# Optimization experiments

Hardware: AMD Instinct MI355X
Metric: run time of the kernel (lower is better)

## Reference

```python
import jax, jax.numpy as jnp
import numpy as np

# Config / sizes
N = 20000       # nodes
E = 320000      # edges (avg degree 16)
IN_DIM = 6      # node feature dim
PE = 8          # laplacian PE dims
ED = 4          # edge feature dim
H = 128         # hidden dim
OUT = 4         # output dim
L = 3           # message-passing layers
T = 3           # node types (typed encoders/decoders)


def mlp(z, W1, b1, W2, b2):
    # _make_mlp: Linear -> ReLU -> Linear
    return jax.nn.relu(z @ W1 + b1) @ W2 + b2


def typed_mlp(z, W1, b1, W2, b2, types):
    # W1: [T, Din, H]; compute all T branches, select per-node by type
    h = jax.nn.relu(jnp.einsum('ni,tih->tnh', z, W1) + b1[:, None, :])
    o = jnp.einsum('tnh,tho->tno', h, W2) + b2[:, None, :]
    onehot = jax.nn.one_hot(types, W1.shape[0], dtype=o.dtype)  # [N, T]
    return jnp.einsum('tno,nt->no', o, onehot)


def setup_inputs() -> dict:
    key = jax.random.key(0)
    ks = jax.random.split(key, 40)

    def w(k, shape, fan_in):
        return jax.random.normal(k, shape, dtype=jnp.float32) / np.float32(np.sqrt(fan_in))

    inp = {}
    inp['x'] = jax.random.normal(ks[0], (N, IN_DIM), dtype=jnp.float32)
    inp['pe'] = jax.random.normal(ks[1], (N, PE), dtype=jnp.float32)
    inp['edge_attr'] = jax.random.normal(ks[2], (E, ED), dtype=jnp.float32)
    # typed node encoders: (in_dim+pe_dims) -> H -> H
    inp['enc_W1'] = w(ks[3], (T, IN_DIM + PE, H), IN_DIM + PE)
    inp['enc_b1'] = jnp.zeros((T, H), jnp.float32)
    inp['enc_W2'] = w(ks[4], (T, H, H), H)
    inp['enc_b2'] = jnp.zeros((T, H), jnp.float32)
    # edge encoder: ED -> H -> H
    inp['ee_W1'] = w(ks[5], (ED, H), ED)
    inp['ee_b1'] = jnp.zeros((H,), jnp.float32)
    inp['ee_W2'] = w(ks[6], (H, H), H)
    inp['ee_b2'] = jnp.zeros((H,), jnp.float32)
    # per-layer edge update (3H->H->H), node update (2H->H->H), fusion (H->H->H)
    inp['eu_W1'] = w(ks[7], (L, 3 * H, H), 3 * H)
    inp['eu_b1'] = jnp.zeros((L, H), jnp.float32)
    inp['eu_W2'] = w(ks[8], (L, H, H), H)
    inp['eu_b2'] = jnp.zeros((L, H), jnp.float32)
    inp['nu_W1'] = w(ks[9], (L, 2 * H, H), 2 * H)
    inp['nu_b1'] = jnp.zeros((L, H), jnp.float32)
    inp['nu_W2'] = w(ks[10], (L, H, H), H)
    inp['nu_b2'] = jnp.zeros((L, H), jnp.float32)
    inp['fu_W1'] = w(ks[11], (L, H, H), H)
    inp['fu_b1'] = jnp.zeros((L, H), jnp.float32)
    inp['fu_W2'] = w(ks[12], (L, H, H), H)
    inp['fu_b2'] = jnp.zeros((L, H), jnp.float32)
    # typed decoders: H -> H -> OUT
    inp['dec_W1'] = w(ks[13], (T, H, H), H)
    inp['dec_b1'] = jnp.zeros((T, H), jnp.float32)
    inp['dec_W2'] = w(ks[14], (T, H, OUT), H)
    inp['dec_b2'] = jnp.zeros((T, OUT), jnp.float32)
    # int inputs
    inp['edge_index'] = jax.random.randint(ks[15], (2, E), 0, N)
    inp['node_types'] = jax.random.randint(ks[16], (N,), 0, T)
    return inp


def reference(x, pe, edge_attr,
              enc_W1, enc_b1, enc_W2, enc_b2,
              ee_W1, ee_b1, ee_W2, ee_b2,
              eu_W1, eu_b1, eu_W2, eu_b2,
              nu_W1, nu_b1, nu_W2, nu_b2,
              fu_W1, fu_b1, fu_W2, fu_b2,
              dec_W1, dec_b1, dec_W2, dec_b2,
              edge_index, node_types):
    n = x.shape[0]
    src, dst = edge_index[0], edge_index[1]
    # typed node encode on [x || pe]
    h_nodes = typed_mlp(jnp.concatenate([x, pe], axis=-1),
                        enc_W1, enc_b1, enc_W2, enc_b2, node_types)
    # edge encode
    h_edges = mlp(edge_attr, ee_W1, ee_b1, ee_W2, ee_b2)
    num_layers = eu_W1.shape[0]
    for l in range(num_layers):
        # gather endpoint states, edge MLP, residual on edges
        m_edge = mlp(jnp.concatenate([h_nodes[src], h_nodes[dst], h_edges], axis=-1),
                     eu_W1[l], eu_b1[l], eu_W2[l], eu_b2[l])
        h_edges = h_edges + m_edge
        # scatter-add aggregation to destination nodes (index_add_)
        m_node = jax.ops.segment_sum(h_edges, dst, num_segments=n)
        # node update + residual, then fusion (dropout is eval/identity)
        upd = mlp(jnp.concatenate([h_nodes, m_node], axis=-1),
                  nu_W1[l], nu_b1[l], nu_W2[l], nu_b2[l])
        local = h_nodes + upd
        h_nodes = mlp(local, fu_W1[l], fu_b1[l], fu_W2[l], fu_b2[l])
    # typed decode
    out = typed_mlp(h_nodes, dec_W1, dec_b1, dec_W2, dec_b2, node_types)
    return out
```

## Files before the change

### kernel.cpp

```cpp
#include <hip/hip_runtime.h>
#include <hip/hip_bf16.h>

typedef __hip_bfloat16 bf16;
typedef __attribute__((ext_vector_type(8))) short short8;
typedef __attribute__((ext_vector_type(4))) float floatx4;

#define HDIM 128
#define NCANON 27

__device__ __forceinline__ float b2f(bf16 v) { return __bfloat162float(v); }
__device__ __forceinline__ float s2f(short s) {
  return __uint_as_float(((unsigned int)(unsigned short)s) << 16);
}
__device__ __forceinline__ short f2s(float f) {
  return (short)__bfloat16_as_ushort(__float2bfloat16(f));
}

struct CanonDesc {
  const void* src[NCANON];
  int prefix[NCANON + 1];
};

__global__ void canon_kernel(CanonDesc d, const unsigned short* __restrict__ xraw,
                             int* __restrict__ flagOut, bf16* __restrict__ out, int total) {
  __shared__ int sflag;
  int tid = threadIdx.x;
  if (tid < 64) {
    unsigned short u = xraw[2 * tid];
    int e = (u >> 7) & 0xFF;
    int ok = (u == 0) || (e >= 100 && e <= 140);
    unsigned long long m = __ballot(ok);
    if (tid == 0) sflag = (__popcll(m) >= 48) ? 1 : 0;
  }
  __syncthreads();
  int isBf = sflag;
  if (blockIdx.x == 0 && tid == 0) flagOut[0] = isBf;
  int t = blockIdx.x * 256 + tid;
  if (t >= total) return;
  int lo = 0, hi = NCANON;
  while (lo + 1 < hi) { int mid = (lo + hi) >> 1; if (d.prefix[mid] <= t) lo = mid; else hi = mid; }
  int off = t - d.prefix[lo];
  out[t] = isBf ? ((const bf16*)d.src[lo])[off]
                : __float2bfloat16(((const float*)d.src[lo])[off]);
}

__global__ void hist_kernel(const int* __restrict__ dst, int* __restrict__ cnt, int E) {
  int e = blockIdx.x * 256 + threadIdx.x;
  if (e < E) atomicAdd(&cnt[dst[e]], 1);
}

__global__ void scan1_kernel(const int* __restrict__ cnt, int* __restrict__ bsum, int n) {
  int tid = threadIdx.x, lane = tid & 63, wave = tid >> 6;
  int i = blockIdx.x * 256 + tid;
  int v = (i < n) ? cnt[i] : 0;
  #pragma unroll
  for (int d = 32; d; d >>= 1) v += __shfl_down(v, d);
  __shared__ int ws[4];
  if (lane == 0) ws[wave] = v;
  __syncthreads();
  if (tid == 0) bsum[blockIdx.x] = ws[0] + ws[1] + ws[2] + ws[3];
}

__global__ void scan2_kernel(int* __restrict__ bsum, int nb) {
  int lane = threadIdx.x;
  int a0 = (lane < nb) ? bsum[lane] : 0;
  int b0 = (64 + lane < nb) ? bsum[64 + lane] : 0;
  int a = a0, b = b0;
  #pragma unroll
  for (int d = 1; d < 64; d <<= 1) { int t = __shfl_up(a, d); if (lane >= d) a += t; }
  int totA = __shfl(a, 63);
  #pragma unroll
  for (int d = 1; d < 64; d <<= 1) { int t = __shfl_up(b, d); if (lane >= d) b += t; }
  int totB = __shfl(b, 63);
  if (lane < nb) bsum[lane] = a - a0;
  if (64 + lane < nb) bsum[64 + lane] = b - b0 + totA;
  if (lane == 0) bsum[nb] = totA + totB;
}

__global__ void scan3_kernel(const int* __restrict__ cnt, const int* __restrict__ bsum,
                             int* __restrict__ row_start, int n, int nb) {
  __shared__ int sh[256];
  int tid = threadIdx.x;
  int i = blockIdx.x * 256 + tid;
  int v = (i < n) ? cnt[i] : 0;
  sh[tid] = v;
  __syncthreads();
  #pragma unroll
  for (int off = 1; off < 256; off <<= 1) {
    int t = (tid >= off) ? sh[tid - off] : 0;
    __syncthreads();
    sh[tid] += t;
    __syncthreads();
  }
  if (i < n) row_start[i] = bsum[blockIdx.x] + sh[tid] - v;
  if (blockIdx.x == 0 && tid == 0) row_start[n] = bsum[nb];
}

__global__ void scatter_kernel(const int* __restrict__ src, const int* __restrict__ dst,
                               const int* __restrict__ row_start, int* __restrict__ cursor,
                               const bf16* __restrict__ ea, bf16* __restrict__ eaS,
                               int* __restrict__ srcS, int* __restrict__ dstS, int E) {
  int e = blockIdx.x * 256 + threadIdx.x;
  if (e < E) {
    int d = dst[e];
    int pos = row_start[d] + atomicAdd(&cursor[d], 1);
    srcS[pos] = src[e];
    dstS[pos] = d;
    *(uint2*)(eaS + (size_t)pos * 4) = *(const uint2*)(ea + (size_t)e * 4);
  }
}

__global__ void __launch_bounds__(1024) tsort_kernel(const int* __restrict__ types,
                                                     int* __restrict__ ts,
                                                     int* __restrict__ perm, int n) {
  __shared__ int wc[16][3];
  __shared__ int base[3];
  int tid = threadIdx.x, lane = tid & 63, wave = tid >> 6;
  int c0 = 0, c1 = 0, c2 = 0;
  for (int i = tid; i < n; i += 1024) {
    int t = types[i];
    c0 += (t == 0); c1 += (t == 1); c2 += (t == 2);
  }
  #pragma unroll
  for (int d = 32; d; d >>= 1) {
    c0 += __shfl_down(c0, d); c1 += __shfl_down(c1, d); c2 += __shfl_down(c2, d);
  }
  if (lane == 0) { wc[wave][0] = c0; wc[wave][1] = c1; wc[wave][2] = c2; }
  __syncthreads();
  if (tid == 0) {
    int t0 = 0, t1 = 0;
    for (int w = 0; w < 16; w++) { t0 += wc[w][0]; t1 += wc[w][1]; }
    ts[0] = 0; ts[1] = t0; ts[2] = t0 + t1; ts[3] = n;
    base[0] = 0; base[1] = t0; base[2] = t0 + t1;
  }
  __syncthreads();
  for (int i0 = 0; i0 < n; i0 += 1024) {
    int i = i0 + tid;
    int t = (i < n) ? types[i] : -1;
    unsigned long long m0 = __ballot(t == 0);
    unsigned long long m1 = __ballot(t == 1);
    unsigned long long m2 = __ballot(t == 2);
    if (lane == 0) { wc[wave][0] = __popcll(m0); wc[wave][1] = __popcll(m1); wc[wave][2] = __popcll(m2); }
    __syncthreads();
    if (i < n) {
      unsigned long long mt = (t == 0) ? m0 : ((t == 1) ? m1 : m2);
      unsigned long long below = (lane == 0) ? 0ull : ((1ull << lane) - 1ull);
      int r = __popcll(mt & below);
      int woff = 0;
      for (int w = 0; w < wave; w++) woff += wc[w][t];
      perm[base[t] + woff + r] = i;
    }
    __syncthreads();
    if (tid == 0) {
      int a0 = 0, a1 = 0, a2 = 0;
      for (int w = 0; w < 16; w++) { a0 += wc[w][0]; a1 += wc[w][1]; a2 += wc[w][2]; }
      base[0] += a0; base[1] += a1; base[2] += a2;
    }
    __syncthreads();
  }
}

struct PackJob { const bf16* src; bf16* dst; int Ksrc; int KS; int srcCols; };
struct PackJobs { PackJob j[40]; };

__global__ void pack_all_kernel(PackJobs J) {
  PackJob job = J.j[blockIdx.y];
  int idx = blockIdx.x * 256 + threadIdx.x;
  int total = 8 * job.KS * 64;
  if (idx >= total) return;
  int lane = idx & 63;
  int ks = (idx >> 6) % job.KS;
  int ct = idx / (64 * job.KS);
  bf16* o = job.dst + (size_t)idx * 8;
  int ncol = ct * 16 + (lane & 15);
  int kb = ks * 32 + ((lane >> 4) & 3) * 8;
  #pragma unroll
  for (int jj = 0; jj < 8; jj++) {
    int k = kb + jj;
    o[jj] = (k < job.Ksrc && ncol < job.srcCols)
              ? job.src[(size_t)k * job.srcCols + ncol] : __float2bfloat16(0.f);
  }
}

__global__ void __launch_bounds__(256) ygemm_kernel(
    const bf16* __restrict__ X,
    const bf16* __restrict__ WpA, const bf16* __restrict__ WpB,
    bf16* __restrict__ outA, bf16* __restrict__ outB,
    float* __restrict__ mnode, int M) {
  const bf16* Wp = blockIdx.y ? WpB : WpA;
  bf16* outp = blockIdx.y ? outB : outA;
  constexpr int BM = 64, RT = 4, SK = 136;
  __shared__ bf16 Zt[BM * SK];
  const int tid = threadIdx.x;
  const int lane = tid & 63, wave = tid >> 6, colq = lane & 15, quad = lane >> 4;
  const int row0 = blockIdx.x * BM;
  if (blockIdx.y == 0) {
    float4 z = {0.f, 0.f, 0.f, 0.f};
    for (int i = tid; i < BM * 32; i += 256) {
      int row = i >> 5, q = i & 31;
      int gr = row0 + row;
      if (gr < M) *(float4*)(mnode + (size_t)gr * HDIM + q * 4) = z;
    }
  }
  {
    int row = tid >> 2, sub = tid & 3;
    int gr = row0 + row;
    bool ok = gr < M;
    #pragma unroll
    for (int j = 0; j < 4; j++) {
      int seg = j * 4 + sub;
      uint4 v = {0u, 0u, 0u, 0u};
// ... 307 lines not shown
    }
  }
  #pragma unroll
  for (int c = 0; c < 2; c++) {
    int col = wave * 32 + c * 16 + colq;
    float bv = b2f(fuB2[col]);
    #pragma unroll
    for (int rt = 0; rt < RT; rt++)
      #pragma unroll
      for (int r = 0; r < 4; r++) {
        int lrow = rt * 16 + quad * 4 + r;
        int grow = row0 + lrow;
        bf16 hb = __float2bfloat16(acc[rt][c][r] + bv);
        Zt[lrow * SK + col] = hb;
        if (grow < M) outp[(size_t)grow * HDIM + col] = hb;
      }
  }
  if (!yW1a) return;
  __syncthreads();

  #pragma unroll
  for (int which = 0; which < 2; which++) {
    const bf16* Wp = which ? yW1b : yW1a;
    bf16* outy = which ? ysB : ysA;
    #pragma unroll
    for (int rt = 0; rt < RT; rt++)
      #pragma unroll
      for (int c = 0; c < 2; c++) acc[rt][c] = (floatx4){0.f, 0.f, 0.f, 0.f};
    #pragma unroll
    for (int ks = 0; ks < 4; ks++) {
      short8 bfr0 = *(const short8*)(Wp + (((size_t)(wave * 2 + 0) * 4 + ks) * 64 + lane) * 8);
      short8 bfr1 = *(const short8*)(Wp + (((size_t)(wave * 2 + 1) * 4 + ks) * 64 + lane) * 8);
      #pragma unroll
      for (int rt = 0; rt < RT; rt++) {
        short8 a = *(const short8*)(&Zt[(rt * 16 + colq) * SK + ks * 32 + quad * 8]);
        acc[rt][0] = __builtin_amdgcn_mfma_f32_16x16x32_bf16(a, bfr0, acc[rt][0], 0, 0, 0);
        acc[rt][1] = __builtin_amdgcn_mfma_f32_16x16x32_bf16(a, bfr1, acc[rt][1], 0, 0, 0);
      }
    }
    #pragma unroll
    for (int c = 0; c < 2; c++) {
      int col = wave * 32 + c * 16 + colq;
      #pragma unroll
      for (int rt = 0; rt < RT; rt++)
        #pragma unroll
        for (int r = 0; r < 4; r++) {
          int grow = row0 + rt * 16 + quad * 4 + r;
          if (grow < M) outy[(size_t)grow * HDIM + col] = __float2bfloat16(acc[rt][c][r]);
        }
    }
  }
}

template<int KS1, bool DEC>
__global__ void __launch_bounds__(256) typed_kernel(
    const bf16* __restrict__ in0, const bf16* __restrict__ in1,
    const int* __restrict__ perm, const int* __restrict__ ts, const int* __restrict__ flagp,
    const bf16* __restrict__ W1p, int w1s, const bf16* __restrict__ b1v, int b1s,
    const bf16* __restrict__ W2p, int w2s, const bf16* __restrict__ b2v, int b2s,
    void* __restrict__ outp) {
  constexpr int BM = 64, RT = 4;
  constexpr int SK = KS1 * 32 + 8;
  constexpr int HS = 136;
  int t = blockIdx.y;
  int rs = ts[t], re = ts[t + 1];
  int row0 = rs + blockIdx.x * BM;
  if (row0 >= re) return;
  __shared__ bf16 Zt[BM * SK];
  __shared__ bf16 Hid[BM * HS];
  __shared__ int gIdx[BM];
  const int tid = threadIdx.x;
  const int lane = tid & 63, wave = tid >> 6, colq = lane & 15, quad = lane >> 4;
  for (int i = tid; i < BM; i += 256) gIdx[i] = (row0 + i < re) ? perm[row0 + i] : -1;
  __syncthreads();
  if (DEC) {
    int row = tid >> 2, sub = tid & 3;
    int g = gIdx[row];
    #pragma unroll
    for (int j = 0; j < 4; j++) {
      int seg = j * 4 + sub;
      uint4 v = {0u, 0u, 0u, 0u};
      if (g >= 0) v = *(const uint4*)(in0 + (size_t)g * HDIM + seg * 8);
      *(uint4*)(&Zt[row * SK + seg * 8]) = v;
    }
  } else {
    for (int i = tid; i < BM * 32; i += 256) {
      int row = i >> 5, k = i & 31;
      int g = gIdx[row];
      bf16 v = __float2bfloat16(0.f);
      if (g >= 0 && k < 14) v = (k < 6) ? in0[(size_t)g * 6 + k] : in1[(size_t)g * 8 + (k - 6)];
      Zt[row * SK + k] = v;
    }
  }
  __syncthreads();

  const bf16* W1t = W1p + (size_t)t * w1s;
  const bf16* W2t = W2p + (size_t)t * w2s;
  floatx4 acc[RT][2];
  #pragma unroll
  for (int rt = 0; rt < RT; rt++)
    #pragma unroll
    for (int c = 0; c < 2; c++) acc[rt][c] = (floatx4){0.f, 0.f, 0.f, 0.f};
  #pragma unroll
  for (int ks = 0; ks < KS1; ks++) {
    short8 bfr0 = *(const short8*)(W1t + (((size_t)(wave * 2 + 0) * KS1 + ks) * 64 + lane) * 8);
    short8 bfr1 = *(const short8*)(W1t + (((size_t)(wave * 2 + 1) * KS1 + ks) * 64 + lane) * 8);
    #pragma unroll
    for (int rt = 0; rt < RT; rt++) {
      short8 a = *(const short8*)(&Zt[(rt * 16 + colq) * SK + ks * 32 + quad * 8]);
      acc[rt][0] = __builtin_amdgcn_mfma_f32_16x16x32_bf16(a, bfr0, acc[rt][0], 0, 0, 0);
      acc[rt][1] = __builtin_amdgcn_mfma_f32_16x16x32_bf16(a, bfr1, acc[rt][1], 0, 0, 0);
    }
  }
  #pragma unroll
  for (int c = 0; c < 2; c++) {
    int col = wave * 32 + c * 16 + colq;
    float bv = b2f(b1v[t * b1s + col]);
    #pragma unroll
    for (int rt = 0; rt < RT; rt++)
      #pragma unroll
      for (int r = 0; r < 4; r++) {
        float v = acc[rt][c][r] + bv;
        Hid[(rt * 16 + quad * 4 + r) * HS + col] = __float2bfloat16(fmaxf(v, 0.f));
      }
  }
  __syncthreads();

  floatx4 acc2[RT][2];
  #pragma unroll
  for (int rt = 0; rt < RT; rt++)
    #pragma unroll
    for (int c = 0; c < 2; c++) acc2[rt][c] = (floatx4){0.f, 0.f, 0.f, 0.f};
  #pragma unroll
  for (int ks = 0; ks < 4; ks++) {
    short8 bfr0 = *(const short8*)(W2t + (((size_t)(wave * 2 + 0) * 4 + ks) * 64 + lane) * 8);
    short8 bfr1 = *(const short8*)(W2t + (((size_t)(wave * 2 + 1) * 4 + ks) * 64 + lane) * 8);
    #pragma unroll
    for (int rt = 0; rt < RT; rt++) {
      short8 a = *(const short8*)(&Hid[(rt * 16 + colq) * HS + ks * 32 + quad * 8]);
      acc2[rt][0] = __builtin_amdgcn_mfma_f32_16x16x32_bf16(a, bfr0, acc2[rt][0], 0, 0, 0);
      acc2[rt][1] = __builtin_amdgcn_mfma_f32_16x16x32_bf16(a, bfr1, acc2[rt][1], 0, 0, 0);
    }
  }
  if (DEC) {
    if (wave == 0 && colq < 4) {
      int isBf = flagp[0];
      float bv = b2f(b2v[t * b2s + colq]);
      #pragma unroll
      for (int rt = 0; rt < RT; rt++)
        #pragma unroll
        for (int r = 0; r < 4; r++) {
          int g = gIdx[rt * 16 + quad * 4 + r];
          if (g >= 0) {
            float v = acc2[rt][0][r] + bv;
            if (isBf) ((bf16*)outp)[(size_t)g * 4 + colq] = __float2bfloat16(v);
            else      ((float*)outp)[(size_t)g * 4 + colq] = v;
          }
        }
    }
  } else {
    #pragma unroll
    for (int c = 0; c < 2; c++) {
      int col = wave * 32 + c * 16 + colq;
      float bv = b2f(b2v[t * b2s + col]);
      #pragma unroll
      for (int rt = 0; rt < RT; rt++)
        #pragma unroll
        for (int r = 0; r < 4; r++) {
          int g = gIdx[rt * 16 + quad * 4 + r];
          if (g >= 0) ((bf16*)outp)[(size_t)g * HDIM + col] = __float2bfloat16(acc2[rt][c][r] + bv);
        }
    }
  }
}

template<int BM>
__global__ void __launch_bounds__(256) ee_kernel(
    const bf16* __restrict__ eaS,
    const bf16* __restrict__ W1p, const bf16* __restrict__ b1v,
    const bf16* __restrict__ W2p, const bf16* __restrict__ b2v,
    bf16* __restrict__ outp, int M) {
  constexpr int RT = BM / 16;
  constexpr int SK = 136;
  __shared__ bf16 Zt[BM * SK];
  const int tid = threadIdx.x;
  const int lane = tid & 63, wave = tid >> 6, colq = lane & 15, quad = lane >> 4;
  const int row0 = blockIdx.x * BM;

  for (int i = tid; i < BM * 4; i += 256) {
    int row = i >> 2, seg = i & 3;
    int gr = row0 + row;
    uint4 val = {0u, 0u, 0u, 0u};
    if (seg == 0 && gr < M) {
      uint2 v = *(const uint2*)(eaS + (size_t)gr * 4);
      val.x = v.x; val.y = v.y;
    }
    *(uint4*)(&Zt[row * SK + seg * 8]) = val;
  }
  __syncthreads();

  floatx4 acc[RT][2];
  #pragma unroll
  for (int rt = 0; rt < RT; rt++)
    #pragma unroll
    for (int c = 0; c < 2; c++) acc[rt][c] = (floatx4){0.f, 0.f, 0.f, 0.f};
  {
    short8 bfr0 = *(const short8*)(W1p + (((size_t)(wave * 2 + 0)) * 64 + lane) * 8);
    short8 bfr1 = *(const short8*)(W1p + (((size_t)(wave * 2 + 1)) * 64 + lane) * 8);
    #pragma unroll
    for (int rt = 0; rt < RT; rt++) {
      short8 a = *(const short8*)(&Zt[(rt * 16 + colq) * SK + quad * 8]);
      acc[rt][0] = __builtin_amdgcn_mfma_f32_16x16x32_bf16(a, bfr0, acc[rt][0], 0, 0, 0);
      acc[rt][1] = __builtin_amdgcn_mfma_f32_16x16x32_bf16(a, bfr1, acc[rt][1], 0, 0, 0);
    }
  }
  __syncthreads();
  #pragma unroll
  for (int c = 0; c < 2; c++) {
    int col = wave * 32 + c * 16 + colq;
    float bv = b2f(b1v[col]);
    #pragma unroll
    for (int rt = 0; rt < RT; rt++)
      #pragma unroll
      for (int r = 0; r < 4; r++)
        Zt[(rt * 16 + quad * 4 + r) * SK + col] =
            __float2bfloat16(fmaxf(acc[rt][c][r] + bv, 0.f));
  }
  __syncthreads();

  floatx4 acc2[RT][2];
  #pragma unroll
  for (int rt = 0; rt < RT; rt++)
    #pragma unroll
    for (int c = 0; c < 2; c++) acc2[rt][c] = (floatx4){0.f, 0.f, 0.f, 0.f};
  #pragma unroll
  for (int ks = 0; ks < 4; ks++) {
    short8 bfr0 = *(const short8*)(W2p + (((size_t)(wave * 2 + 0) * 4 + ks) * 64 + lane) * 8);
    short8 bfr1 = *(const short8*)(W2p + (((size_t)(wave * 2 + 1) * 4 + ks) * 64 + lane) * 8);
    #pragma unroll
    for (int rt = 0; rt < RT; rt++) {
      short8 a = *(const short8*)(&Zt[(rt * 16 + colq) * SK + ks * 32 + quad * 8]);
      acc2[rt][0] = __builtin_amdgcn_mfma_f32_16x16x32_bf16(a, bfr0, acc2[rt][0], 0, 0, 0);
      acc2[rt][1] = __builtin_amdgcn_mfma_f32_16x16x32_bf16(a, bfr1, acc2[rt][1], 0, 0, 0);
    }
  }
  #pragma unroll
  for (int c = 0; c < 2; c++) {
    int col = wave * 32 + c * 16 + colq;
    float bv = b2f(b2v[col]);
    #pragma unroll
    for (int rt = 0; rt < RT; rt++)
      #pragma unroll
      for (int r = 0; r < 4; r++) {
        int grow = row0 + rt * 16 + quad * 4 + r;
        if (grow < M)
          outp[(size_t)grow * HDIM + col] = __float2bfloat16(acc2[rt][c][r] + bv);
      }
  }
}

extern "C" void kernel_launch(void* const* d_in, const int* in_sizes, int n_in,
                              void* d_out, int out_size, void* d_ws, size_t ws_size,
                              hipStream_t stream) {
  const int* edge_index = (const int*)d_in[27];
  const int* node_types = (const int*)d_in[28];
  const int N = in_sizes[28];
  const int E = in_sizes[2] / 4;
  const int L = in_sizes[12] / HDIM;
  const int* srcI = edge_index;
  const int* dstI = edge_index + E;

  CanonDesc cd;
  int total = 0;
  for (int i = 0; i < NCANON; i++) { cd.src[i] = d_in[i]; cd.prefix[i] = total; total += in_sizes[i]; }
  cd.prefix[NCANON] = total;

  char* wsb = (char*)d_ws;
  size_t off = 0;
  auto alloc = [&](size_t bytes) -> void* {
    void* p = wsb + off;
    off += (bytes + 255) & ~(size_t)255;
    return p;
  };
  int*  flag      = (int*)alloc(256);
  bf16* arena     = (bf16*)alloc((size_t)total * 2);
  bf16* h_nodes   = (bf16*)alloc((size_t)N * HDIM * 2);
  bf16* h_edges   = (bf16*)alloc((size_t)E * HDIM * 2);
  float* m_node   = (float*)alloc((size_t)N * HDIM * 4);
  bf16* ysrcb     = (bf16*)alloc((size_t)N * HDIM * 2);
  bf16* ydstb     = (bf16*)alloc((size_t)N * HDIM * 2);
  bf16* eaS       = (bf16*)alloc((size_t)E * 4 * 2);
  int* counts     = (int*)alloc((size_t)N * 4);
  int* cursor     = (int*)alloc((size_t)N * 4);
  int* row_start  = (int*)alloc((size_t)(N + 1) * 4);
  int* bsum       = (int*)alloc(260 * 4);
  int* srcS       = (int*)alloc((size_t)E * 4);
  int* dstS       = (int*)alloc((size_t)E * 4);
  int* tsArr      = (int*)alloc(64);
  int* permT      = (int*)alloc((size_t)N * 4);
  bf16* eeW1p  = (bf16*)alloc(4096 * 2);
  bf16* eeW2p  = (bf16*)alloc(16384 * 2);
  bf16* encW1p = (bf16*)alloc(3 * 4096 * 2);
  bf16* encW2p = (bf16*)alloc(3 * 16384 * 2);
  bf16* decW1p = (bf16*)alloc(3 * 16384 * 2);
  bf16* decW2p = (bf16*)alloc(3 * 16384 * 2);
  bf16* euW1a  = (bf16*)alloc((size_t)L * 16384 * 2);
  bf16* euW1b  = (bf16*)alloc((size_t)L * 16384 * 2);
  bf16* euW1c  = (bf16*)alloc((size_t)L * 16384 * 2);
  bf16* euW2p  = (bf16*)alloc((size_t)L * 16384 * 2);
  bf16* nuW1p  = (bf16*)alloc((size_t)L * 32768 * 2);
  bf16* nuW2p  = (bf16*)alloc((size_t)L * 16384 * 2);
  bf16* fuW1p  = (bf16*)alloc((size_t)L * 16384 * 2);
  bf16* fuW2p  = (bf16*)alloc((size_t)L * 16384 * 2);

  const bf16* cX     = arena + cd.prefix[0];
  const bf16* cPE    = arena + cd.prefix[1];
  const bf16* cEA    = arena + cd.prefix[2];
  const bf16* cEncW1 = arena + cd.prefix[3];
  const bf16* cEncB1 = arena + cd.prefix[4];
  const bf16* cEncW2 = arena + cd.prefix[5];
  const bf16* cEncB2 = arena + cd.prefix[6];
  const bf16* cEeW1  = arena + cd.prefix[7];
  const bf16* cEeB1  = arena + cd.prefix[8];
  const bf16* cEeW2  = arena + cd.prefix[9];
  const bf16* cEeB2  = arena + cd.prefix[10];
  const bf16* cEuW1  = arena + cd.prefix[11];
  const bf16* cEuB1  = arena + cd.prefix[12];
  const bf16* cEuW2  = arena + cd.prefix[13];
  const bf16* cEuB2  = arena + cd.prefix[14];
  const bf16* cNuW1  = arena + cd.prefix[15];
  const bf16* cNuB1  = arena + cd.prefix[16];
  const bf16* cNuW2  = arena + cd.prefix[17];
  const bf16* cNuB2  = arena + cd.prefix[18];
  const bf16* cFuW1  = arena + cd.prefix[19];
  const bf16* cFuB1  = arena + cd.prefix[20];
  const bf16* cFuW2  = arena + cd.prefix[21];
  const bf16* cFuB2  = arena + cd.prefix[22];
  const bf16* cDecW1 = arena + cd.prefix[23];
  const bf16* cDecB1 = arena + cd.prefix[24];
  const bf16* cDecW2 = arena + cd.prefix[25];
  const bf16* cDecB2 = arena + cd.prefix[26];

  canon_kernel<<<(total + 255) / 256, 256, 0, stream>>>(
      cd, (const unsigned short*)d_in[0], flag, arena, total);

  hipMemsetAsync(counts, 0, (size_t)N * 4, stream);
  hipMemsetAsync(cursor, 0, (size_t)N * 4, stream);

  PackJobs PJ;
  int nj = 0;
  PJ.j[nj++] = {cEeW1, eeW1p, 4, 1, 128};
  PJ.j[nj++] = {cEeW2, eeW2p, 128, 4, 128};
  for (int l = 0; l < L; l++) {
    const bf16* w1 = cEuW1 + (size_t)l * 384 * HDIM;
    PJ.j[nj++] = {w1,                 euW1a + (size_t)l * 16384, 128, 4, 128};
    PJ.j[nj++] = {w1 + 128 * HDIM,    euW1b + (size_t)l * 16384, 128, 4, 128};
    PJ.j[nj++] = {w1 + 256 * HDIM,    euW1c + (size_t)l * 16384, 128, 4, 128};
    PJ.j[nj++] = {cEuW2 + (size_t)l * HDIM * HDIM, euW2p + (size_t)l * 16384, 128, 4, 128};
    PJ.j[nj++] = {cNuW1 + (size_t)l * 256 * HDIM,  nuW1p + (size_t)l * 32768, 256, 8, 128};
    PJ.j[nj++] = {cNuW2 + (size_t)l * HDIM * HDIM, nuW2p + (size_t)l * 16384, 128, 4, 128};
    PJ.j[nj++] = {cFuW1 + (size_t)l * HDIM * HDIM, fuW1p + (size_t)l * 16384, 128, 4, 128};
    PJ.j[nj++] = {cFuW2 + (size_t)l * HDIM * HDIM, fuW2p + (size_t)l * 16384, 128, 4, 128};
  }
  for (int t = 0; t < 3; t++) {
    PJ.j[nj++] = {cEncW1 + (size_t)t * 14 * HDIM,   encW1p + (size_t)t * 4096, 14, 1, 128};
    PJ.j[nj++] = {cEncW2 + (size_t)t * HDIM * HDIM, encW2p + (size_t)t * 16384, 128, 4, 128};
    PJ.j[nj++] = {cDecW1 + (size_t)t * HDIM * HDIM, decW1p + (size_t)t * 16384, 128, 4, 128};
    PJ.j[nj++] = {cDecW2 + (size_t)t * HDIM * 4,    decW2p + (size_t)t * 16384, 128, 4, 4};
  }
  pack_all_kernel<<<dim3(16, nj), 256, 0, stream>>>(PJ);

  int nb = (N + 255) / 256;
  hist_kernel<<<(E + 255) / 256, 256, 0, stream>>>(dstI, counts, E);
  scan1_kernel<<<nb, 256, 0, stream>>>(counts, bsum, N);
  scan2_kernel<<<1, 64, 0, stream>>>(bsum, nb);
  scan3_kernel<<<nb, 256, 0, stream>>>(counts, bsum, row_start, N, nb);
  scatter_kernel<<<(E + 255) / 256, 256, 0, stream>>>(srcI, dstI, row_start, cursor,
                                                      cEA, eaS, srcS, dstS, E);
  tsort_kernel<<<1, 1024, 0, stream>>>(node_types, tsArr, permT, N);

  int ngrid64 = (N + 63) / 64;
  typed_kernel<1, false><<<dim3(ngrid64, 3), 256, 0, stream>>>(
      cX, cPE, permT, tsArr, flag, encW1p, 4096, cEncB1, HDIM,
      encW2p, 16384, cEncB2, HDIM, h_nodes);

  int egrid32  = (E + 31) / 32;
  int egrid128 = (E + 127) / 128;

  ee_kernel<128><<<egrid128, 256, 0, stream>>>(
      eaS, eeW1p, cEeB1, eeW2p, cEeB2, h_edges, E);

  for (int l = 0; l < L; l++) {
    if (l == 0) {
      ygemm_kernel<<<dim3(ngrid64, 2), 256, 0, stream>>>(
          h_nodes, euW1a, euW1b, ysrcb, ydstb, m_node, N);
    }
    if (l + 1 < L) {
      eu_kernel<32, true><<<egrid32, 256, 0, stream>>>(
          h_edges, ysrcb, ydstb, srcS, dstS,
          euW1c + (size_t)l * 16384, cEuB1 + l * HDIM,
          euW2p + (size_t)l * 16384, cEuB2 + l * HDIM, h_edges, m_node, E);
    } else {
      eu_kernel<32, false><<<egrid32, 256, 0, stream>>>(
          h_edges, ysrcb, ydstb, srcS, dstS,
          euW1c + (size_t)l * 16384, cEuB1 + l * HDIM,
          euW2p + (size_t)l * 16384, cEuB2 + l * HDIM, h_edges, m_node, E);
    }
    bool hasNext = (l + 1 < L);
    node_kernel<<<ngrid64, 256, 0, stream>>>(
        h_nodes, m_node,
        nuW1p + (size_t)l * 32768, cNuB1 + l * HDIM,
        nuW2p + (size_t)l * 16384, cNuB2 + l * HDIM,
        fuW1p + (size_t)l * 16384, cFuB1 + l * HDIM,
        fuW2p + (size_t)l * 16384, cFuB2 + l * HDIM,
        hasNext ? euW1a + (size_t)(l + 1) * 16384 : nullptr,
        hasNext ? euW1b + (size_t)(l + 1) * 16384 : nullptr,
        ysrcb, ydstb, h_nodes, N);
  }

  typed_kernel<4, true><<<dim3(ngrid64, 3), 256, 0, stream>>>(
      h_nodes, nullptr, permT, tsArr, flag, decW1p, 16384, cDecB1, HDIM,
      decW2p, 16384, cDecB2, 4, d_out);
  (void)n_in; (void)ws_size;
}
```

Baseline: 476.2 us.

## Merge small setup kernels to cut launch count and dead work

Folds the memsets of counts and cursor into extra blocks of the canon kernel, merges the histogram with the type-sort kernel, and merges the edge encoder with the typed node encoder into one launch by splitting on block index. The decoder gets its own kernel whose second GEMM computes only the single 16-column tile that holds the 4 outputs, instead of 8 tiles where most were discarded. The aim is to remove launch gaps and serialization between small kernels, at the cost of more complex, branchy kernels. The zeroing relies on counts and cursor sitting contiguously in the workspace, and the large shared array in the merged encoder kernel may lower occupancy for the node-encode blocks.

```diff
diff --git a/kernel.cpp b/kernel.cpp
--- a/kernel.cpp
+++ b/kernel.cpp
@@ -22,9 +22,15 @@
 };
 
 __global__ void canon_kernel(CanonDesc d, const unsigned short* __restrict__ xraw,
-                             int* __restrict__ flagOut, bf16* __restrict__ out, int total) {
+                             int* __restrict__ flagOut, bf16* __restrict__ out, int total,
+                             int canonBlocks, uint4* __restrict__ zbase, int zquads) {
+  int tid = threadIdx.x;
+  if (blockIdx.x >= canonBlocks) {
+    int i = (blockIdx.x - canonBlocks) * 256 + tid;
+    if (i < zquads) { uint4 z = {0u, 0u, 0u, 0u}; zbase[i] = z; }
+    return;
+  }
   __shared__ int sflag;
-  int tid = threadIdx.x;
   if (tid < 64) {
     unsigned short u = xraw[2 * tid];
     int e = (u >> 7) & 0xFF;
@@ -44,75 +50,14 @@
                 : __float2bfloat16(((const float*)d.src[lo])[off]);
 }
 
-__global__ void hist_kernel(const int* __restrict__ dst, int* __restrict__ cnt, int E) {
-  int e = blockIdx.x * 256 + threadIdx.x;
-  if (e < E) atomicAdd(&cnt[dst[e]], 1);
-}
-
-__global__ void scan1_kernel(const int* __restrict__ cnt, int* __restrict__ bsum, int n) {
-  int tid = threadIdx.x, lane = tid & 63, wave = tid >> 6;
-  int i = blockIdx.x * 256 + tid;
-  int v = (i < n) ? cnt[i] : 0;
-  #pragma unroll
-  for (int d = 32; d; d >>= 1) v += __shfl_down(v, d);
-  __shared__ int ws[4];
-  if (lane == 0) ws[wave] = v;
-  __syncthreads();
-  if (tid == 0) bsum[blockIdx.x] = ws[0] + ws[1] + ws[2] + ws[3];
-}
-
-__global__ void scan2_kernel(int* __restrict__ bsum, int nb) {
-  int lane = threadIdx.x;
-  int a0 = (lane < nb) ? bsum[lane] : 0;
-  int b0 = (64 + lane < nb) ? bsum[64 + lane] : 0;
-  int a = a0, b = b0;
-  #pragma unroll
-  for (int d = 1; d < 64; d <<= 1) { int t = __shfl_up(a, d); if (lane >= d) a += t; }
-  int totA = __shfl(a, 63);
-  #pragma unroll
-  for (int d = 1; d < 64; d <<= 1) { int t = __shfl_up(b, d); if (lane >= d) b += t; }
-  int totB = __shfl(b, 63);
-  if (lane < nb) bsum[lane] = a - a0;
-  if (64 + lane < nb) bsum[64 + lane] = b - b0 + totA;
-  if (lane == 0) bsum[nb] = totA + totB;
-}
-
-__global__ void scan3_kernel(const int* __restrict__ cnt, const int* __restrict__ bsum,
-                             int* __restrict__ row_start, int n, int nb) {
-  __shared__ int sh[256];
-  int tid = threadIdx.x;
-  int i = blockIdx.x * 256 + tid;
-  int v = (i < n) ? cnt[i] : 0;
-  sh[tid] = v;
-  __syncthreads();
-  #pragma unroll
-  for (int off = 1; off < 256; off <<= 1) {
-    int t = (tid >= off) ? sh[tid - off] : 0;
-    __syncthreads();
-    sh[tid] += t;
-    __syncthreads();
-  }
-  if (i < n) row_start[i] = bsum[blockIdx.x] + sh[tid] - v;
-  if (blockIdx.x == 0 && tid == 0) row_start[n] = bsum[nb];
-}
-
-__global__ void scatter_kernel(const int* __restrict__ src, const int* __restrict__ dst,
-                               const int* __restrict__ row_start, int* __restrict__ cursor,
-                               const bf16* __restrict__ ea, bf16* __restrict__ eaS,
-                               int* __restrict__ srcS, int* __restrict__ dstS, int E) {
-  int e = blockIdx.x * 256 + threadIdx.x;
-  if (e < E) {
-    int d = dst[e];
-    int pos = row_start[d] + atomicAdd(&cursor[d], 1);
-    srcS[pos] = src[e];
-    dstS[pos] = d;
-    *(uint2*)(eaS + (size_t)pos * 4) = *(const uint2*)(ea + (size_t)e * 4);
-  }
-}
-
-__global__ void __launch_bounds__(1024) tsort_kernel(const int* __restrict__ types,
-                                                     int* __restrict__ ts,
-                                                     int* __restrict__ perm, int n) {
+__global__ void __launch_bounds__(1024) hist_tsort_kernel(
+    const int* __restrict__ dst, int* __restrict__ cnt, int E, int hb,
+    const int* __restrict__ types, int* __restrict__ ts, int* __restrict__ perm, int n) {
+  if (blockIdx.x < hb) {
+    int e = blockIdx.x * 1024 + threadIdx.x;
+    if (e < E) atomicAdd(&cnt[dst[e]], 1);
+    return;
+  }
   __shared__ int wc[16][3];
   __shared__ int base[3];
   int tid = threadIdx.x, lane = tid & 63, wave = tid >> 6;
@@ -157,6 +102,67 @@
       base[0] += a0; base[1] += a1; base[2] += a2;
     }
     __syncthreads();
+  }
+}
+
+__global__ void scan1_kernel(const int* __restrict__ cnt, int* __restrict__ bsum, int n) {
+  int tid = threadIdx.x, lane = tid & 63, wave = tid >> 6;
+  int i = blockIdx.x * 256 + tid;
+  int v = (i < n) ? cnt[i] : 0;
+  #pragma unroll
+  for (int d = 32; d; d >>= 1) v += __shfl_down(v, d);
+  __shared__ int ws[4];
+  if (lane == 0) ws[wave] = v;
+  __syncthreads();
+  if (tid == 0) bsum[blockIdx.x] = ws[0] + ws[1] + ws[2] + ws[3];
+}
+
+__global__ void scan2_kernel(int* __restrict__ bsum, int nb) {
+  int lane = threadIdx.x;
+  int a0 = (lane < nb) ? bsum[lane] : 0;
+  int b0 = (64 + lane < nb) ? bsum[64 + lane] : 0;
+  int a = a0, b = b0;
+  #pragma unroll
+  for (int d = 1; d < 64; d <<= 1) { int t = __shfl_up(a, d); if (lane >= d) a += t; }
+  int totA = __shfl(a, 63);
+  #pragma unroll
+  for (int d = 1; d < 64; d <<= 1) { int t = __shfl_up(b, d); if (lane >= d) b += t; }
+  int totB = __shfl(b, 63);
+  if (lane < nb) bsum[lane] = a - a0;
+  if (64 + lane < nb) bsum[64 + lane] = b - b0 + totA;
+  if (lane == 0) bsum[nb] = totA + totB;
+}
+
+__global__ void scan3_kernel(const int* __restrict__ cnt, const int* __restrict__ bsum,
+                             int* __restrict__ row_start, int n, int nb) {
+  __shared__ int sh[256];
+  int tid = threadIdx.x;
+  int i = blockIdx.x * 256 + tid;
+  int v = (i < n) ? cnt[i] : 0;
+  sh[tid] = v;
+  __syncthreads();
+  #pragma unroll
+  for (int off = 1; off < 256; off <<= 1) {
+    int t = (tid >= off) ? sh[tid - off] : 0;
+    __syncthreads();
+    sh[tid] += t;
+    __syncthreads();
+  }
+  if (i < n) row_start[i] = bsum[blockIdx.x] + sh[tid] - v;
+  if (blockIdx.x == 0 && tid == 0) row_start[n] = bsum[nb];
+}
+
+__global__ void scatter_kernel(const int* __restrict__ src, const int* __restrict__ dst,
+                               const int* __restrict__ row_start, int* __restrict__ cursor,
+                               const bf16* __restrict__ ea, bf16* __restrict__ eaS,
+                               int* __restrict__ srcS, int* __restrict__ dstS, int E) {
+  int e = blockIdx.x * 256 + threadIdx.x;
+  if (e < E) {
+    int d = dst[e];
+    int pos = row_start[d] + atomicAdd(&cursor[d], 1);
+    srcS[pos] = src[e];
+    dstS[pos] = d;
+    *(uint2*)(eaS + (size_t)pos * 4) = *(const uint2*)(ea + (size_t)e * 4);
   }
 }
 
@@ -570,16 +576,184 @@
   }
 }
 
-template<int KS1, bool DEC>
-__global__ void __launch_bounds__(256) typed_kernel(
-    const bf16* __restrict__ in0, const bf16* __restrict__ in1,
+__global__ void __launch_bounds__(256) encee_kernel(
+    int eeBlocks, int ngrid64,
+    const bf16* __restrict__ eaS,
+    const bf16* __restrict__ eeW1, const bf16* __restrict__ eeB1,
+    const bf16* __restrict__ eeW2, const bf16* __restrict__ eeB2,
+    bf16* __restrict__ h_edges, int E,
+    const bf16* __restrict__ x, const bf16* __restrict__ pe,
+    const int* __restrict__ perm, const int* __restrict__ ts,
+    const bf16* __restrict__ encW1, const bf16* __restrict__ encB1,
+    const bf16* __restrict__ encW2, const bf16* __restrict__ encB2,
+    bf16* __restrict__ h_nodes) {
+  __shared__ bf16 smem[128 * 136];
+  __shared__ int gIdx[64];
+  const int tid = threadIdx.x;
+  const int lane = tid & 63, wave = tid >> 6, colq = lane & 15, quad = lane >> 4;
+
+  if (blockIdx.x < eeBlocks) {
+    constexpr int BM = 128, RT = 8, SK = 136;
+    bf16* Zt = smem;
+    const int row0 = blockIdx.x * BM;
+    for (int i = tid; i < BM * 4; i += 256) {
+      int row = i >> 2, seg = i & 3;
+      int gr = row0 + row;
+      uint4 val = {0u, 0u, 0u, 0u};
+      if (seg == 0 && gr < E) {
+        uint2 v = *(const uint2*)(eaS + (size_t)gr * 4);
+        val.x = v.x; val.y = v.y;
+      }
+      *(uint4*)(&Zt[row * SK + seg * 8]) = val;
+    }
+    __syncthreads();
+    floatx4 acc[RT][2];
+    #pragma unroll
+    for (int rt = 0; rt < RT; rt++)
+      #pragma unroll
+      for (int c = 0; c < 2; c++) acc[rt][c] = (floatx4){0.f, 0.f, 0.f, 0.f};
+    {
+      short8 bfr0 = *(const short8*)(eeW1 + (((size_t)(wave * 2 + 0)) * 64 + lane) * 8);
+      short8 bfr1 = *(const short8*)(eeW1 + (((size_t)(wave * 2 + 1)) * 64 + lane) * 8);
+      #pragma unroll
+      for (int rt = 0; rt < RT; rt++) {
+        short8 a = *(const short8*)(&Zt[(rt * 16 + colq) * SK + quad * 8]);
+        acc[rt][0] = __builtin_amdgcn_mfma_f32_16x16x32_bf16(a, bfr0, acc[rt][0], 0, 0, 0);
+        acc[rt][1] = __builtin_amdgcn_mfma_f32_16x16x32_bf16(a, bfr1, acc[rt][1], 0, 0, 0);
+      }
+    }
+    __syncthreads();
+    #pragma unroll
+    for (int c = 0; c < 2; c++) {
+      int col = wave * 32 + c * 16 + colq;
+      float bv = b2f(eeB1[col]);
+      #pragma unroll
+      for (int rt = 0; rt < RT; rt++)
+        #pragma unroll
+        for (int r = 0; r < 4; r++)
+          Zt[(rt * 16 + quad * 4 + r) * SK + col] =
+              __float2bfloat16(fmaxf(acc[rt][c][r] + bv, 0.f));
+    }
+    __syncthreads();
+    floatx4 acc2[RT][2];
+    #pragma unroll
+    for (int rt = 0; rt < RT; rt++)
+      #pragma unroll
+      for (int c = 0; c < 2; c++) acc2[rt][c] = (floatx4){0.f, 0.f, 0.f, 0.f};
+    #pragma unroll
+    for (int ks = 0; ks < 4; ks++) {
+      short8 bfr0 = *(const short8*)(eeW2 + (((size_t)(wave * 2 + 0) * 4 + ks) * 64 + lane) * 8);
+      short8 bfr1 = *(const short8*)(eeW2 + (((size_t)(wave * 2 + 1) * 4 + ks) * 64 + lane) * 8);
+      #pragma unroll
+      for (int rt = 0; rt < RT; rt++) {
+        short8 a = *(const short8*)(&Zt[(rt * 16 + colq) * SK + ks * 32 + quad * 8]);
+        acc2[rt][0] = __builtin_amdgcn_mfma_f32_16x16x32_bf16(a, bfr0, acc2[rt][0], 0, 0, 0);
+        acc2[rt][1] = __builtin_amdgcn_mfma_f32_16x16x32_bf16(a, bfr1, acc2[rt][1], 0, 0, 0);
+      }
+    }
+    #pragma unroll
+    for (int c = 0; c < 2; c++) {
+      int col = wave * 32 + c * 16 + colq;
+      float bv = b2f(eeB2[col]);
+      #pragma unroll
+      for (int rt = 0; rt < RT; rt++)
+        #pragma unroll
+        for (int r = 0; r < 4; r++) {
+          int grow = row0 + rt * 16 + quad * 4 + r;
+          if (grow < E)
+            h_edges[(size_t)grow * HDIM + col] = __float2bfloat16(acc2[rt][c][r] + bv);
+        }
+    }
+    return;
+  }
+
+  {
+    constexpr int BM = 64, RT = 4, SK = 40, HS = 136;
+    bf16* Zt = smem;
+    bf16* Hid = smem + BM * SK;
+    int idx = blockIdx.x - eeBlocks;
+    int t = idx / ngrid64;
+    int bx = idx - t * ngrid64;
+    int rs = ts[t], re = ts[t + 1];
+    int row0 = rs + bx * BM;
+    if (row0 >= re) return;
+    for (int i = tid; i < BM; i += 256) gIdx[i] = (row0 + i < re) ? perm[row0 + i] : -1;
+    __syncthreads();
+    for (int i = tid; i < BM * 32; i += 256) {
+      int row = i >> 5, k = i & 31;
+      int g = gIdx[row];
+      bf16 v = __float2bfloat16(0.f);
+      if (g >= 0 && k < 14) v = (k < 6) ? x[(size_t)g * 6 + k] : pe[(size_t)g * 8 + (k - 6)];
+      Zt[row * SK + k] = v;
+    }
+    __syncthreads();
+    const bf16* W1t = encW1 + (size_t)t * 4096;
+    const bf16* W2t = encW2 + (size_t)t * 16384;
+    floatx4 acc[RT][2];
+    #pragma unroll
+    for (int rt = 0; rt < RT; rt++)
+      #pragma unroll
+      for (int c = 0; c < 2; c++) acc[rt][c] = (floatx4){0.f, 0.f, 0.f, 0.f};
+    {
+      short8 bfr0 = *(const short8*)(W1t + (((size_t)(wave * 2 + 0)) * 64 + lane) * 8);
+      short8 bfr1 = *(const short8*)(W1t + (((size_t)(wave * 2 + 1)) * 64 + lane) * 8);
+      #pragma unroll
+      for (int rt = 0; rt < RT; rt++) {
+        short8 a = *(const short8*)(&Zt[(rt * 16 + colq) * SK + quad * 8]);
+        acc[rt][0] = __builtin_amdgcn_mfma_f32_16x16x32_bf16(a, bfr0, acc[rt][0], 0, 0, 0);
+        acc[rt][1] = __builtin_amdgcn_mfma_f32_16x16x32_bf16(a, bfr1, acc[rt][1], 0, 0, 0);
+      }
+    }
+    #pragma unroll
+    for (int c = 0; c < 2; c++) {
+      int col = wave * 32 + c * 16 + colq;
+      float bv = b2f(encB1[t * HDIM + col]);
+      #pragma unroll
+      for (int rt = 0; rt < RT; rt++)
+        #pragma unroll
+        for (int r = 0; r < 4; r++)
+          Hid[(rt * 16 + quad * 4 + r) * HS + col] =
+              __float2bfloat16(fmaxf(acc[rt][c][r] + bv, 0.f));
+    }
+    __syncthreads();
+    floatx4 acc2[RT][2];
+    #pragma unroll
+    for (int rt = 0; rt < RT; rt++)
+      #pragma unroll
+      for (int c = 0; c < 2; c++) acc2[rt][c] = (floatx4){0.f, 0.f, 0.f, 0.f};
+    #pragma unroll
+    for (int ks = 0; ks < 4; ks++) {
+      short8 bfr0 = *(const short8*)(W2t + (((size_t)(wave * 2 + 0) * 4 + ks) * 64 + lane) * 8);
+      short8 bfr1 = *(const short8*)(W2t + (((size_t)(wave * 2 + 1) * 4 + ks) * 64 + lane) * 8);
+      #pragma unroll
+      for (int rt = 0; rt < RT; rt++) {
+        short8 a = *(const short8*)(&Hid[(rt * 16 + colq) * HS + ks * 32 + quad * 8]);
+        acc2[rt][0] = __builtin_amdgcn_mfma_f32_16x16x32_bf16(a, bfr0, acc2[rt][0], 0, 0, 0);
+        acc2[rt][1] = __builtin_amdgcn_mfma_f32_16x16x32_bf16(a, bfr1, acc2[rt][1], 0, 0, 0);
+      }
+    }
+    #pragma unroll
+    for (int c = 0; c < 2; c++) {
+      int col = wave * 32 + c * 16 + colq;
+      float bv = b2f(encB2[t * HDIM + col]);
+      #pragma unroll
+      for (int rt = 0; rt < RT; rt++)
+        #pragma unroll
+        for (int r = 0; r < 4; r++) {
+          int g = gIdx[rt * 16 + quad * 4 + r];
+          if (g >= 0) h_nodes[(size_t)g * HDIM + col] = __float2bfloat16(acc2[rt][c][r] + bv);
+        }
+    }
+  }
+}
+
+__global__ void __launch_bounds__(256) dec_kernel(
+    const bf16* __restrict__ in0,
     const int* __restrict__ perm, const int* __restrict__ ts, const int* __restrict__ flagp,
-    const bf16* __restrict__ W1p, int w1s, const bf16* __restrict__ b1v, int b1s,
-    const bf16* __restrict__ W2p, int w2s, const bf16* __restrict__ b2v, int b2s,
+    const bf16* __restrict__ W1p, const bf16* __restrict__ b1v,
+    const bf16* __restrict__ W2p, const bf16* __restrict__ b2v,
     void* __restrict__ outp) {
-  constexpr int BM = 64, RT = 4;
-  constexpr int SK = KS1 * 32 + 8;
-  constexpr int HS = 136;
+  constexpr int BM = 64, RT = 4, SK = 136, HS = 136;
   int t = blockIdx.y;
   int rs = ts[t], re = ts[t + 1];
   int row0 = rs + blockIdx.x * BM;
@@ -591,7 +765,7 @@
   const int lane = tid & 63, wave = tid >> 6, colq = lane & 15, quad = lane >> 4;
   for (int i = tid; i < BM; i += 256) gIdx[i] = (row0 + i < re) ? perm[row0 + i] : -1;
   __syncthreads();
-  if (DEC) {
+  {
     int row = tid >> 2, sub = tid & 3;
     int g = gIdx[row];
     #pragma unroll
@@ -601,28 +775,19 @@
       if (g >= 0) v = *(const uint4*)(in0 + (size_t)g * HDIM + seg * 8);
       *(uint4*)(&Zt[row * SK + seg * 8]) = v;
     }
-  } else {
-    for (int i = tid; i < BM * 32; i += 256) {
-      int row = i >> 5, k = i & 31;
-      int g = gIdx[row];
-      bf16 v = __float2bfloat16(0.f);
-      if (g >= 0 && k < 14) v = (k < 6) ? in0[(size_t)g * 6 + k] : in1[(size_t)g * 8 + (k - 6)];
-      Zt[row * SK + k] = v;
-    }
-  }
-  __syncthreads();
-
-  const bf16* W1t = W1p + (size_t)t * w1s;
-  const bf16* W2t = W2p + (size_t)t * w2s;
+  }
+  __syncthreads();
+  const bf16* W1t = W1p + (size_t)t * 16384;
+  const bf16* W2t = W2p + (size_t)t * 16384;
   floatx4 acc[RT][2];
   #pragma unroll
   for (int rt = 0; rt < RT; rt++)
     #pragma unroll
     for (int c = 0; c < 2; c++) acc[rt][c] = (floatx4){0.f, 0.f, 0.f, 0.f};
   #pragma unroll
-  for (int ks = 0; ks < KS1; ks++) {
-    short8 bfr0 = *(const short8*)(W1t + (((size_t)(wave * 2 + 0) * KS1 + ks) * 64 + lane) * 8);
-    short8 bfr1 = *(const short8*)(W1t + (((size_t)(wave * 2 + 1) * KS1 + ks) * 64 + lane) * 8);
+  for (int ks = 0; ks < 4; ks++) {
+    short8 bfr0 = *(const short8*)(W1t + (((size_t)(wave * 2 + 0) * 4 + ks) * 64 + lane) * 8);
+    short8 bfr1 = *(const short8*)(W1t + (((size_t)(wave * 2 + 1) * 4 + ks) * 64 + lane) * 8);
     #pragma unroll
     for (int rt = 0; rt < RT; rt++) {
       short8 a = *(const short8*)(&Zt[(rt * 16 + colq) * SK + ks * 32 + quad * 8]);
@@ -633,146 +798,40 @@
   #pragma unroll
   for (int c = 0; c < 2; c++) {
     int col = wave * 32 + c * 16 + colq;
-    float bv = b2f(b1v[t * b1s + col]);
-    #pragma unroll
-    for (int rt = 0; rt < RT; rt++)
-      #pragma unroll
-      for (int r = 0; r < 4; r++) {
-        float v = acc[rt][c][r] + bv;
-        Hid[(rt * 16 + quad * 4 + r) * HS + col] = __float2bfloat16(fmaxf(v, 0.f));
-      }
-  }
-  __syncthreads();
-
-  floatx4 acc2[RT][2];
-  #pragma unroll
-  for (int rt = 0; rt < RT; rt++)
-    #pragma unroll
-    for (int c = 0; c < 2; c++) acc2[rt][c] = (floatx4){0.f, 0.f, 0.f, 0.f};
+    float bv = b2f(b1v[t * HDIM + col]);
+    #pragma unroll
+    for (int rt = 0; rt < RT; rt++)
+      #pragma unroll
+      for (int r = 0; r < 4; r++)
+        Hid[(rt * 16 + quad * 4 + r) * HS + col] =
+            __float2bfloat16(fmaxf(acc[rt][c][r] + bv, 0.f));
+  }
+  __syncthreads();
+  floatx4 acc2[RT];
+  #pragma unroll
+  for (int rt = 0; rt < RT; rt++) acc2[rt] = (floatx4){0.f, 0.f, 0.f, 0.f};
   #pragma unroll
   for (int ks = 0; ks < 4; ks++) {
-    short8 bfr0 = *(const short8*)(W2t + (((size_t)(wave * 2 + 0) * 4 + ks) * 64 + lane) * 8);
-    short8 bfr1 = *(const short8*)(W2t + (((size_t)(wave * 2 + 1) * 4 + ks) * 64 + lane) * 8);
+    short8 bfr0 = *(const short8*)(W2t + (((size_t)0 * 4 + ks) * 64 + lane) * 8);
     #pragma unroll
     for (int rt = 0; rt < RT; rt++) {
       short8 a = *(const short8*)(&Hid[(rt * 16 + colq) * HS + ks * 32 + quad * 8]);
-      acc2[rt][0] = __builtin_amdgcn_mfma_f32_16x16x32_bf16(a, bfr0, acc2[rt][0], 0, 0, 0);
-      acc2[rt][1] = __builtin_amdgcn_mfma_f32_16x16x32_bf16(a, bfr1, acc2[rt][1], 0, 0, 0);
-    }
-  }
-  if (DEC) {
-    if (wave == 0 && colq < 4) {
-      int isBf = flagp[0];
-      float bv = b2f(b2v[t * b2s + colq]);
-      #pragma unroll
-      for (int rt = 0; rt < RT; rt++)
-        #pragma unroll
-        for (int r = 0; r < 4; r++) {
-          int g = gIdx[rt * 16 + quad * 4 + r];
-          if (g >= 0) {
-            float v = acc2[rt][0][r] + bv;
-            if (isBf) ((bf16*)outp)[(size_t)g * 4 + colq] = __float2bfloat16(v);
-            else      ((float*)outp)[(size_t)g * 4 + colq] = v;
-          }
+      acc2[rt] = __builtin_amdgcn_mfma_f32_16x16x32_bf16(a, bfr0, acc2[rt], 0, 0, 0);
+    }
+  }
+  if (wave == 0 && colq < 4) {
+    int isBf = flagp[0];
+    float bv = b2f(b2v[t * 4 + colq]);
+    #pragma unroll
+    for (int rt = 0; rt < RT; rt++)
+      #pragma unroll
+      for (int r = 0; r < 4; r++) {
+        int g = gIdx[rt * 16 + quad * 4 + r];
+        if (g >= 0) {
+          float v = acc2[rt][r] + bv;
+          if (isBf) ((bf16*)outp)[(size_t)g * 4 + colq] = __float2bfloat16(v);
+          else      ((float*)outp)[(size_t)g * 4 + colq] = v;
         }
-    }
-  } else {
-    #pragma unroll
-    for (int c = 0; c < 2; c++) {
-      int col = wave * 32 + c * 16 + colq;
-      float bv = b2f(b2v[t * b2s + col]);
-      #pragma unroll
-      for (int rt = 0; rt < RT; rt++)
-        #pragma unroll
-        for (int r = 0; r < 4; r++) {
-          int g = gIdx[rt * 16 + quad * 4 + r];
-          if (g >= 0) ((bf16*)outp)[(size_t)g * HDIM + col] = __float2bfloat16(acc2[rt][c][r] + bv);
-        }
-    }
-  }
-}
-
-template<int BM>
-__global__ void __launch_bounds__(256) ee_kernel(
-    const bf16* __restrict__ eaS,
-    const bf16* __restrict__ W1p, const bf16* __restrict__ b1v,
-    const bf16* __restrict__ W2p, const bf16* __restrict__ b2v,
-    bf16* __restrict__ outp, int M) {
-  constexpr int RT = BM / 16;
-  constexpr int SK = 136;
-  __shared__ bf16 Zt[BM * SK];
-  const int tid = threadIdx.x;
-  const int lane = tid & 63, wave = tid >> 6, colq = lane & 15, quad = lane >> 4;
-  const int row0 = blockIdx.x * BM;
-
-  for (int i = tid; i < BM * 4; i += 256) {
-    int row = i >> 2, seg = i & 3;
-    int gr = row0 + row;
-    uint4 val = {0u, 0u, 0u, 0u};
-    if (seg == 0 && gr < M) {
-      uint2 v = *(const uint2*)(eaS + (size_t)gr * 4);
-      val.x = v.x; val.y = v.y;
-    }
-    *(uint4*)(&Zt[row * SK + seg * 8]) = val;
-  }
-  __syncthreads();
-
-  floatx4 acc[RT][2];
-  #pragma unroll
-  for (int rt = 0; rt < RT; rt++)
-    #pragma unroll
-    for (int c = 0; c < 2; c++) acc[rt][c] = (floatx4){0.f, 0.f, 0.f, 0.f};
-  {
-    short8 bfr0 = *(const short8*)(W1p + (((size_t)(wave * 2 + 0)) * 64 + lane) * 8);
-    short8 bfr1 = *(const short8*)(W1p + (((size_t)(wave * 2 + 1)) * 64 + lane) * 8);
-    #pragma unroll
-    for (int rt = 0; rt < RT; rt++) {
-      short8 a = *(const short8*)(&Zt[(rt * 16 + colq) * SK + quad * 8]);
-      acc[rt][0] = __builtin_amdgcn_mfma_f32_16x16x32_bf16(a, bfr0, acc[rt][0], 0, 0, 0);
-      acc[rt][1] = __builtin_amdgcn_mfma_f32_16x16x32_bf16(a, bfr1, acc[rt][1], 0, 0, 0);
-    }
-  }
-  __syncthreads();
-  #pragma unroll
-  for (int c = 0; c < 2; c++) {
-    int col = wave * 32 + c * 16 + colq;
-    float bv = b2f(b1v[col]);
-    #pragma unroll
-    for (int rt = 0; rt < RT; rt++)
-      #pragma unroll
-      for (int r = 0; r < 4; r++)
-        Zt[(rt * 16 + quad * 4 + r) * SK + col] =
-            __float2bfloat16(fmaxf(acc[rt][c][r] + bv, 0.f));
-  }
-  __syncthreads();
-
-  floatx4 acc2[RT][2];
-  #pragma unroll
-  for (int rt = 0; rt < RT; rt++)
-    #pragma unroll
-    for (int c = 0; c < 2; c++) acc2[rt][c] = (floatx4){0.f, 0.f, 0.f, 0.f};
-  #pragma unroll
-  for (int ks = 0; ks < 4; ks++) {
-    short8 bfr0 = *(const short8*)(W2p + (((size_t)(wave * 2 + 0) * 4 + ks) * 64 + lane) * 8);
-    short8 bfr1 = *(const short8*)(W2p + (((size_t)(wave * 2 + 1) * 4 + ks) * 64 + lane) * 8);
-    #pragma unroll
-    for (int rt = 0; rt < RT; rt++) {
-      short8 a = *(const short8*)(&Zt[(rt * 16 + colq) * SK + ks * 32 + quad * 8]);
-      acc2[rt][0] = __builtin_amdgcn_mfma_f32_16x16x32_bf16(a, bfr0, acc2[rt][0], 0, 0, 0);
-      acc2[rt][1] = __builtin_amdgcn_mfma_f32_16x16x32_bf16(a, bfr1, acc2[rt][1], 0, 0, 0);
-    }
-  }
-  #pragma unroll
-  for (int c = 0; c < 2; c++) {
-    int col = wave * 32 + c * 16 + colq;
-    float bv = b2f(b2v[col]);
-    #pragma unroll
-    for (int rt = 0; rt < RT; rt++)
-      #pragma unroll
-      for (int r = 0; r < 4; r++) {
-        int grow = row0 + rt * 16 + quad * 4 + r;
-        if (grow < M)
-          outp[(size_t)grow * HDIM + col] = __float2bfloat16(acc2[rt][c][r] + bv);
       }
   }
 }
@@ -859,11 +918,17 @@
   const bf16* cDecW2 = arena + cd.prefix[25];
   const bf16* cDecB2 = arena + cd.prefix[26];
 
-  canon_kernel<<<(total + 255) / 256, 256, 0, stream>>>(
-      cd, (const unsigned short*)d_in[0], flag, arena, total);
-
-  hipMemsetAsync(counts, 0, (size_t)N * 4, stream);
-  hipMemsetAsync(cursor, 0, (size_t)N * 4, stream);
+  int canonBlocks = (total + 255) / 256;
+  size_t zbytes = (size_t)((char*)cursor - (char*)counts) + (size_t)N * 4;
+  int zquads = (int)(zbytes / 16);
+  int zBlocks = (zquads + 255) / 256;
+  canon_kernel<<<canonBlocks + zBlocks, 256, 0, stream>>>(
+      cd, (const unsigned short*)d_in[0], flag, arena, total, canonBlocks,
+      (uint4*)counts, zquads);
+
+  int hb = (E + 1023) / 1024;
+  hist_tsort_kernel<<<hb + 1, 1024, 0, stream>>>(dstI, counts, E, hb,
+                                                 node_types, tsArr, permT, N);
 
   PackJobs PJ;
   int nj = 0;
@@ -889,24 +954,20 @@
   pack_all_kernel<<<dim3(16, nj), 256, 0, stream>>>(PJ);
 
   int nb = (N + 255) / 256;
-  hist_kernel<<<(E + 255) / 256, 256, 0, stream>>>(dstI, counts, E);
   scan1_kernel<<<nb, 256, 0, stream>>>(counts, bsum, N);
   scan2_kernel<<<1, 64, 0, stream>>>(bsum, nb);
   scan3_kernel<<<nb, 256, 0, stream>>>(counts, bsum, row_start, N, nb);
   scatter_kernel<<<(E + 255) / 256, 256, 0, stream>>>(srcI, dstI, row_start, cursor,
                                                       cEA, eaS, srcS, dstS, E);
-  tsort_kernel<<<1, 1024, 0, stream>>>(node_types, tsArr, permT, N);
-
-  int ngrid64 = (N + 63) / 64;
-  typed_kernel<1, false><<<dim3(ngrid64, 3), 256, 0, stream>>>(
-      cX, cPE, permT, tsArr, flag, encW1p, 4096, cEncB1, HDIM,
-      encW2p, 16384, cEncB2, HDIM, h_nodes);
-
+
+  int ngrid64  = (N + 63) / 64;
   int egrid32  = (E + 31) / 32;
   int egrid128 = (E + 127) / 128;
 
-  ee_kernel<128><<<egrid128, 256, 0, stream>>>(
-      eaS, eeW1p, cEeB1, eeW2p, cEeB2, h_edges, E);
+  encee_kernel<<<egrid128 + 3 * ngrid64, 256, 0, stream>>>(
+      egrid128, ngrid64,
+      eaS, eeW1p, cEeB1, eeW2p, cEeB2, h_edges, E,
+      cX, cPE, permT, tsArr, encW1p, cEncB1, encW2p, cEncB2, h_nodes);
 
   for (int l = 0; l < L; l++) {
     if (l == 0) {
@@ -936,8 +997,7 @@
         ysrcb, ydstb, h_nodes, N);
   }
 
-  typed_kernel<4, true><<<dim3(ngrid64, 3), 256, 0, stream>>>(
-      h_nodes, nullptr, permT, tsArr, flag, decW1p, 16384, cDecB1, HDIM,
-      decW2p, 16384, cDecB2, 4, d_out);
+  dec_kernel<<<dim3(ngrid64, 3), 256, 0, stream>>>(
+      h_nodes, permT, tsArr, flag, decW1p, cDecB1, decW2p, cDecB2, d_out);
   (void)n_in; (void)ws_size;
 }
```

After: 474.6 us. Within noise of the previous version (-0.3%).
